# Kernel optimization log

Measured on AMD Instinct MI355X. Metric: run time of the kernel, lower is better.

Reference implementation:

```python
import jax, jax.numpy as jnp
import numpy as np
import math

D_MODEL = 1024
N_HEAD = 16
HEAD_DIM = D_MODEL // N_HEAD
D_FF = 4096
NUM_STEPS = 100.0
RESCALE = 4000.0
EPS = 1e-5


def _sin_emb(t):
    # SinusoidalPosEmb: t scaled by rescale_steps/num_steps
    half = D_MODEL // 2
    x = t.astype(jnp.float32) / NUM_STEPS * RESCALE
    freqs = jnp.exp(jnp.arange(half, dtype=jnp.float32) * (-math.log(10000.0) / (half - 1)))
    e = x[:, None] * freqs[None, :]
    return jnp.concatenate([jnp.sin(e), jnp.cos(e)], axis=-1)


def _ln(x):
    m = jnp.mean(x, axis=-1, keepdims=True)
    v = jnp.var(x, axis=-1, keepdims=True)
    return (x - m) / jnp.sqrt(v + EPS)


def _gelu2(x):
    return x * jax.nn.sigmoid(1.702 * x)


def setup_inputs() -> dict:
    key = jax.random.key(0)
    ks = jax.random.split(key, 24)
    B, S, D, F = 4, 512, D_MODEL, D_FF
    std = 0.02
    inp = {
        'src': jax.random.normal(ks[0], (B, S, D), dtype=jnp.float32),
        'src_mask': jax.random.randint(ks[1], (B, 1, S, S), 0, 2).astype(bool),
        'timestep': jax.random.randint(ks[2], (B,), 0, 100, dtype=jnp.int32),
        'attention_bias': jax.random.normal(ks[3], (B, N_HEAD, S, S), dtype=jnp.float32),
        # AdaLayerNorm linear: D -> 2D (scale, shift)
        'W_ada': jax.random.normal(ks[4], (D, 2 * D), dtype=jnp.float32) * std,
        'b_ada': jnp.zeros((2 * D,), dtype=jnp.float32),
        'Wq': jax.random.normal(ks[5], (D, D), dtype=jnp.float32) * std,
        'bq': jnp.zeros((D,), dtype=jnp.float32),
        'Wk': jax.random.normal(ks[6], (D, D), dtype=jnp.float32) * std,
        'bk': jnp.zeros((D,), dtype=jnp.float32),
        'Wv': jax.random.normal(ks[7], (D, D), dtype=jnp.float32) * std,
        'bv': jnp.zeros((D,), dtype=jnp.float32),
        'Wo': jax.random.normal(ks[8], (D, D), dtype=jnp.float32) * std,
        'bo': jnp.zeros((D,), dtype=jnp.float32),
        'W1': jax.random.normal(ks[9], (D, F), dtype=jnp.float32) * std,
        'b1': jnp.zeros((F,), dtype=jnp.float32),
        'W2': jax.random.normal(ks[10], (F, D), dtype=jnp.float32) * std,
        'b2': jnp.zeros((D,), dtype=jnp.float32),
        'g2': jnp.ones((D,), dtype=jnp.float32),
        'beta2': jnp.zeros((D,), dtype=jnp.float32),
    }
    return inp


def reference(src, src_mask, timestep, attention_bias, W_ada, b_ada,
              Wq, bq, Wk, bk, Wv, bv, Wo, bo, W1, b1, W2, b2, g2, beta2):
    B, S, D = src.shape
    # AdaLayerNorm: LN(x) * (1 + scale) + shift, scale/shift from timestep emb
    emb = jax.nn.silu(_sin_emb(timestep)) @ W_ada + b_ada  # [B, 2D]
    scale, shift = jnp.split(emb[:, None, :], 2, axis=-1)  # each [B,1,D]
    x = _ln(src) * (1.0 + scale) + shift

    # Self-attention with spatial bias + fp32 masked softmax
    q = (x @ Wq + bq).reshape(B, S, N_HEAD, HEAD_DIM).transpose(0, 2, 1, 3)
    k = (x @ Wk + bk).reshape(B, S, N_HEAD, HEAD_DIM).transpose(0, 2, 1, 3)
    v = (x @ Wv + bv).reshape(B, S, N_HEAD, HEAD_DIM).transpose(0, 2, 1, 3)
    scores = jnp.einsum('bhqd,bhkd->bhqk', q / math.sqrt(HEAD_DIM), k)
    scores = scores + attention_bias
    scores = jnp.where(src_mask, -jnp.inf, scores.astype(jnp.float32))
    probs = jax.nn.softmax(scores, axis=-1).astype(v.dtype)
    ctx = jnp.einsum('bhqk,bhkd->bhqd', probs, v)
    ctx = ctx.transpose(0, 2, 1, 3).reshape(B, S, D)
    x = x + (ctx @ Wo + bo)  # residual from AdaLN output (as in source)

    # FFN with gelu2 on LN2(x)
    h = _ln(x) * g2 + beta2
    ff = _gelu2(h @ W1 + b1) @ W2 + b2
    return x + ff
```

## Files before the change

### kernel.cpp

```cpp
#include <hip/hip_runtime.h>
#include <math.h>

typedef __bf16 bf16x8 __attribute__((ext_vector_type(8)));
typedef float  f32x4  __attribute__((ext_vector_type(4)));
typedef unsigned short u16x8 __attribute__((ext_vector_type(8)));

__device__ __forceinline__ float bf2f(unsigned short u) {
    return __uint_as_float(((unsigned int)u) << 16);
}
__device__ __forceinline__ unsigned short f2bf_n(float f) {
    return __builtin_bit_cast(unsigned short, (__bf16)f);
}

#define BATCH 4
#define SEQ 512
#define DM 1024
#define NH 16
#define DH 64
#define DFF 4096
#define MROWS (BATCH * SEQ)

__global__ __launch_bounds__(256) void fill0_kernel(float* __restrict__ out) {
    out[blockIdx.x * 256 + threadIdx.x] = 0.0f;
}

__global__ __launch_bounds__(256) void tconv_kernel(const float* __restrict__ in,
                                                    unsigned short* __restrict__ out,
                                                    int K, int N) {
    __shared__ float tile[64][33];
    const int n0 = blockIdx.x * 32, k0 = blockIdx.y * 64;
    const int t = threadIdx.x;
    const int tx = t & 31, ty = t >> 5;
    #pragma unroll
    for (int i = 0; i < 8; ++i)
        tile[ty + i * 8][tx] = in[(size_t)(k0 + ty + i * 8) * N + n0 + tx];
    __syncthreads();
    const int nr = t >> 3;
    const int ks = (t & 7) * 8;
    u16x8 v;
    #pragma unroll
    for (int j = 0; j < 8; ++j) v[j] = f2bf_n(tile[ks + j][nr]);
    *(u16x8*)&out[(size_t)(n0 + nr) * K + k0 + ks] = v;
}

__global__ __launch_bounds__(256) void tconv4_kernel(const float* __restrict__ i0,
                                                     const float* __restrict__ i1,
                                                     const float* __restrict__ i2,
                                                     const float* __restrict__ i3,
                                                     unsigned short* __restrict__ o0,
                                                     unsigned short* __restrict__ o1,
                                                     unsigned short* __restrict__ o2,
                                                     unsigned short* __restrict__ o3) {
    const int z = blockIdx.z;
    const float* in = (z == 0) ? i0 : (z == 1) ? i1 : (z == 2) ? i2 : i3;
    unsigned short* out = (z == 0) ? o0 : (z == 1) ? o1 : (z == 2) ? o2 : o3;
    __shared__ float tile[64][33];
    const int n0 = blockIdx.x * 32, k0 = blockIdx.y * 64;
    const int t = threadIdx.x;
    const int tx = t & 31, ty = t >> 5;
    #pragma unroll
    for (int i = 0; i < 8; ++i)
        tile[ty + i * 8][tx] = in[(size_t)(k0 + ty + i * 8) * 1024 + n0 + tx];
    __syncthreads();
    const int nr = t >> 3;
    const int ks = (t & 7) * 8;
    u16x8 v;
    #pragma unroll
    for (int j = 0; j < 8; ++j) v[j] = f2bf_n(tile[ks + j][nr]);
    *(u16x8*)&out[(size_t)(n0 + nr) * 1024 + k0 + ks] = v;
}

__global__ void semb_kernel(const int* __restrict__ ts, float* __restrict__ semb) {
    int b = blockIdx.x;
    float x = (float)ts[b] * 40.0f;
    for (int j = threadIdx.x; j < 1024; j += 256) {
        int idx = (j < 512) ? j : (j - 512);
        float fr = expf(-9.210340371976184f * (float)idx / 511.0f);
        float e = x * fr;
        float v = (j < 512) ? sinf(e) : cosf(e);
        semb[b * 1024 + j] = v / (1.0f + expf(-v));
    }
}

__global__ __launch_bounds__(256) void ada_part_kernel(const float* __restrict__ semb,
                                                       const float* __restrict__ W,
                                                       float* __restrict__ part) {
    const int nb = blockIdx.x, kc = blockIdx.y;
    const int t = threadIdx.x;
    __shared__ float e_s[4][64];
    e_s[t >> 6][t & 63] = semb[(t >> 6) * 1024 + kc * 64 + (t & 63)];
    __syncthreads();
    const int n = nb * 128 + (t & 127);
    const int half = t >> 7;
    float a0 = 0.f, a1 = 0.f, a2 = 0.f, a3 = 0.f;
    const int kk0 = half * 32;
    #pragma unroll 8
    for (int kk = kk0; kk < kk0 + 32; ++kk) {
        const float w = W[(size_t)(kc * 64 + kk) * 2048 + n];
        a0 += e_s[0][kk] * w; a1 += e_s[1][kk] * w;
        a2 += e_s[2][kk] * w; a3 += e_s[3][kk] * w;
    }
    const int j = kc * 2 + half;
    float* p = part + (size_t)j * 4 * 2048 + n;
    p[0] = a0; p[2048] = a1; p[2 * 2048] = a2; p[3 * 2048] = a3;
}

__global__ __launch_bounds__(256) void ada_red_kernel(const float* __restrict__ part,
                                                      const float* __restrict__ bias,
                                                      float* __restrict__ ss) {
    const int idx = blockIdx.x * 256 + threadIdx.x;
    const int b = idx >> 11, n = idx & 2047;
    float acc = bias[n];
    #pragma unroll 8
    for (int j = 0; j < 32; ++j) acc += part[((size_t)j * 4 + b) * 2048 + n];
    ss[b * 2048 + n] = acc;
}

__global__ __launch_bounds__(256) void adaln_kernel(const float* __restrict__ src,
                                                    const float* __restrict__ ss,
                                                    unsigned short* __restrict__ xb) {
    int r = blockIdx.x;
    int b = r >> 9;
    int t = threadIdx.x;
    float4 v4 = *reinterpret_cast<const float4*>(&src[(size_t)r * DM + t * 4]);
    float v[4] = {v4.x, v4.y, v4.z, v4.w};
    float s = v[0] + v[1] + v[2] + v[3];
    float q = v[0]*v[0] + v[1]*v[1] + v[2]*v[2] + v[3]*v[3];
    #pragma unroll
    for (int off = 32; off > 0; off >>= 1) { s += __shfl_down(s, off); q += __shfl_down(q, off); }
    __shared__ float red[8];
    if ((t & 63) == 0) { red[t >> 6] = s; red[4 + (t >> 6)] = q; }
    __syncthreads();
    s = red[0] + red[1] + red[2] + red[3];
    q = red[4] + red[5] + red[6] + red[7];
    float mean = s * (1.0f / DM);
    float var = q * (1.0f / DM) - mean * mean;
    float rstd = rsqrtf(var + 1e-5f);
    ushort4 o;
    o.x = f2bf_n((v[0]-mean)*rstd*(1.0f+ss[b*2048 + t*4+0]) + ss[b*2048+1024 + t*4+0]);
    o.y = f2bf_n((v[1]-mean)*rstd*(1.0f+ss[b*2048 + t*4+1]) + ss[b*2048+1024 + t*4+1]);
    o.z = f2bf_n((v[2]-mean)*rstd*(1.0f+ss[b*2048 + t*4+2]) + ss[b*2048+1024 + t*4+2]);
    o.w = f2bf_n((v[3]-mean)*rstd*(1.0f+ss[b*2048 + t*4+3]) + ss[b*2048+1024 + t*4+3]);
    *reinterpret_cast<ushort4*>(&xb[(size_t)r * DM + t * 4]) = o;
}

__global__ __launch_bounds__(256) void ln2_kernel(const unsigned short* __restrict__ x,
                                                  const float* __restrict__ g2,
                                                  const float* __restrict__ beta2,
                                                  unsigned short* __restrict__ hout) {
    int r = blockIdx.x;
    int t = threadIdx.x;
    ushort4 s4 = *reinterpret_cast<const ushort4*>(&x[(size_t)r * DM + t * 4]);
    float v[4] = {bf2f(s4.x), bf2f(s4.y), bf2f(s4.z), bf2f(s4.w)};
    float s = v[0] + v[1] + v[2] + v[3];
    float q = v[0]*v[0] + v[1]*v[1] + v[2]*v[2] + v[3]*v[3];
    #pragma unroll
    for (int off = 32; off > 0; off >>= 1) { s += __shfl_down(s, off); q += __shfl_down(q, off); }
    __shared__ float red[8];
    if ((t & 63) == 0) { red[t >> 6] = s; red[4 + (t >> 6)] = q; }
    __syncthreads();
    s = red[0] + red[1] + red[2] + red[3];
    q = red[4] + red[5] + red[6] + red[7];
    float mean = s * (1.0f / DM);
    float var = q * (1.0f / DM) - mean * mean;
    float rstd = rsqrtf(var + 1e-5f);
    ushort4 o;
    o.x = f2bf_n((v[0]-mean)*rstd*g2[t*4+0] + beta2[t*4+0]);
    o.y = f2bf_n((v[1]-mean)*rstd*g2[t*4+1] + beta2[t*4+1]);
    o.z = f2bf_n((v[2]-mean)*rstd*g2[t*4+2] + beta2[t*4+2]);
    o.w = f2bf_n((v[3]-mean)*rstd*g2[t*4+3] + beta2[t*4+3]);
    *reinterpret_cast<ushort4*>(&hout[(size_t)r * DM + t * 4]) = o;
}

#define TBM 64
#define TBN 128
#define TBK 64
#define PIT 68

template<int MODE>
__global__ __launch_bounds__(256) void gemm_bt(
    const unsigned short* __restrict__ A,
    const unsigned short* __restrict__ Wta, const unsigned short* __restrict__ Wtb,
    const unsigned short* __restrict__ Wtc,
    const float* __restrict__ ba, const float* __restrict__ bbb, const float* __restrict__ bc,
    const unsigned short* __restrict__ resid,
    unsigned short* __restrict__ oa, unsigned short* __restrict__ ob,
    unsigned short* __restrict__ oc,
    float* __restrict__ outF,
    int M, int N, int K, int ldk)
{
    const int gx = gridDim.x, gy = gridDim.y;
    const int nwg = gx * gy * gridDim.z;
    const int wid = blockIdx.x + gx * (blockIdx.y + gy * blockIdx.z);
    const int aid = (wid & 7) * (nwg >> 3) + (wid >> 3);
    const int plane = gx * gy;
    const int sel = aid / plane;
    const int pid = aid % plane;
    const int by = pid % gy;
    const int bx = pid / gy;

    const unsigned short* Wt = (sel == 0) ? Wta : (sel == 1) ? Wtb : Wtc;
    const float* bias = (sel == 0) ? ba : (sel == 1) ? bbb : bc;
    unsigned short* outB = (sel == 0) ? oa : (sel == 1) ? ob : oc;

    __shared__ unsigned short As[2][TBM * PIT];
    __shared__ unsigned short Bs[2][TBN * PIT];
    const int t = threadIdx.x;
    const int lane = t & 63;
    const int w = t >> 6, wm = w >> 1, wn = w & 1;
    const int l15 = lane & 15, l4 = lane >> 4;
    const int m0 = by * TBM, n0 = bx * TBN;

    f32x4 acc[2][4];
    #pragma unroll
    for (int i = 0; i < 2; ++i)
        #pragma unroll
        for (int j = 0; j < 4; ++j)
            #pragma unroll
            for (int r = 0; r < 4; ++r) acc[i][j][r] = 0.0f;

    const int ar = t >> 2, aseg = (t & 3) * 16;
    const unsigned short* aG = A + (size_t)(m0 + ar) * K + aseg;
    const int aLo = ar * PIT + aseg;
    const int br = t >> 1, bseg = (t & 1) * 32;
    const unsigned short* bG = Wt + (size_t)(n0 + br) * ldk + bseg;
    const int bLo = br * PIT + bseg;

    u16x8 ra0 = *(const u16x8*)(aG);
    u16x8 ra1 = *(const u16x8*)(aG + 8);
    u16x8 rb0 = *(const u16x8*)(bG);
    u16x8 rb1 = *(const u16x8*)(bG + 8);
    u16x8 rb2 = *(const u16x8*)(bG + 16);
    u16x8 rb3 = *(const u16x8*)(bG + 24);
    *(u16x8*)&As[0][aLo] = ra0; *(u16x8*)&As[0][aLo + 8] = ra1;
    *(u16x8*)&Bs[0][bLo] = rb0; *(u16x8*)&Bs[0][bLo + 8] = rb1;
    *(u16x8*)&Bs[0][bLo + 16] = rb2; *(u16x8*)&Bs[0][bLo + 24] = rb3;
    __syncthreads();

    const int NT = K / TBK;
    for (int kt = 0; kt < NT; ++kt) {
        const int cur = kt & 1;
        const bool more = (kt + 1 < NT);
        if (more) {
            const int k0 = (kt + 1) * TBK;
            ra0 = *(const u16x8*)(aG + k0);
            ra1 = *(const u16x8*)(aG + k0 + 8);
            rb0 = *(const u16x8*)(bG + k0);
            rb1 = *(const u16x8*)(bG + k0 + 8);
            rb2 = *(const u16x8*)(bG + k0 + 16);
            rb3 = *(const u16x8*)(bG + k0 + 24);
        }
        #pragma unroll
        for (int kk = 0; kk < 2; ++kk) {
            bf16x8 af[2], bfr[4];
            #pragma unroll
            for (int mt = 0; mt < 2; ++mt) {
                u16x8 tmp = *(const u16x8*)&As[cur][(wm*32 + mt*16 + l15) * PIT + kk*32 + l4*8];
                af[mt] = __builtin_bit_cast(bf16x8, tmp);
            }
            #pragma unroll
            for (int nt = 0; nt < 4; ++nt) {
                u16x8 tmp = *(const u16x8*)&Bs[cur][(wn*64 + nt*16 + l15) * PIT + kk*32 + l4*8];
                bfr[nt] = __builtin_bit_cast(bf16x8, tmp);
            }
            #pragma unroll
            for (int mt = 0; mt < 2; ++mt)
                #pragma unroll
                for (int nt = 0; nt < 4; ++nt)
                    acc[mt][nt] = __builtin_amdgcn_mfma_f32_16x16x32_bf16(
                        af[mt], bfr[nt], acc[mt][nt], 0, 0, 0);
        }
        if (more) {
            const int nx = cur ^ 1;
            *(u16x8*)&As[nx][aLo] = ra0; *(u16x8*)&As[nx][aLo + 8] = ra1;
            *(u16x8*)&Bs[nx][bLo] = rb0; *(u16x8*)&Bs[nx][bLo + 8] = rb1;
            *(u16x8*)&Bs[nx][bLo + 16] = rb2; *(u16x8*)&Bs[nx][bLo + 24] = rb3;
            __syncthreads();
        }
    }

    #pragma unroll
    for (int mt = 0; mt < 2; ++mt) {
        const int mbase = m0 + wm*32 + mt*16 + l4*4;
        #pragma unroll
        for (int nt = 0; nt < 4; ++nt) {
            const int n = n0 + wn*64 + nt*16 + l15;
            const float bs = (MODE == 4) ? 0.0f : bias[n];
            #pragma unroll
            for (int r = 0; r < 4; ++r) {
                const int m = mbase + r;
                float v = acc[mt][nt][r] + bs;
                if (MODE == 2) v = v / (1.0f + expf(-1.702f * v));
                if (MODE == 1 || MODE == 3) v += bf2f(resid[(size_t)m * N + n]);
                if (MODE == 3)      outF[(size_t)m * N + n] = v;
                else if (MODE == 4) outF[(size_t)m * N + n] += v;
                else                outB[(size_t)m * N + n] = f2bf_n(v);
            }
        }
    }
}

#define QB2 32
#define AKT 64
#define KROW 72
#define VROW 72
#define PROW 72
#define SBPIT 72

__global__ __launch_bounds__(128) void attn_mfma(const unsigned short* __restrict__ qbuf,
                                                 const unsigned short* __restrict__ kbuf,
                                                 const unsigned short* __restrict__ vbuf,
                                                 const float* __restrict__ attb,
                                                 const int* __restrict__ mask,
                                                 unsigned short* __restrict__ ctx) {
    __shared__ unsigned short Ks[AKT * KROW];
    __shared__ unsigned short Vt[DH * VROW];
    __shared__ unsigned short Pb[2 * 16 * PROW];
    __shared__ unsigned short Sb[QB2 * SBPIT];
    const int t = threadIdx.x;
    const int lane = t & 63;
    const int w = t >> 6;
    const int l15 = lane & 15, l4 = lane >> 4;
    const int q0 = blockIdx.x * QB2;
    const int h = blockIdx.y;
    const int b = blockIdx.z;

    bf16x8 qf[2];
    {
        const unsigned short* qrow = qbuf + ((size_t)(b * SEQ + q0 + w * 16 + l15)) * DM + h * DH;
        u16x8 t0 = *(const u16x8*)(qrow + l4 * 8);
        u16x8 t1 = *(const u16x8*)(qrow + 32 + l4 * 8);
        qf[0] = __builtin_bit_cast(bf16x8, t0);
        qf[1] = __builtin_bit_cast(bf16x8, t1);
    }

    float m[4] = {-1e30f, -1e30f, -1e30f, -1e30f};
    float l[4] = {0.0f, 0.0f, 0.0f, 0.0f};
    f32x4 o[4];
    #pragma unroll
    for (int dt = 0; dt < 4; ++dt)
        #pragma unroll
        for (int r = 0; r < 4; ++r) o[dt][r] = 0.0f;

    unsigned short* Pw = Pb + w * 16 * PROW;

    const int kr = t >> 1, c0 = (t & 1) * 32;
    const int kp = t & 31, vg = t >> 5;

    u16x8 rk0, rk1, rk2, rk3, rv0, rv1, rv2, rv3;
    float4 rb[4];
    int4   rm[4];

#define LOADT(KT) {                                                                     \
    const int kbase = (KT) * AKT;                                                       \
    const unsigned short* gk = kbuf + ((size_t)(b * SEQ + kbase + kr)) * DM + h * DH + c0; \
    rk0 = *(const u16x8*)gk;        rk1 = *(const u16x8*)(gk + 8);                      \
    rk2 = *(const u16x8*)(gk + 16); rk3 = *(const u16x8*)(gk + 24);                     \
    const unsigned short* gv = vbuf + ((size_t)(b * SEQ + kbase + 2 * kp)) * DM + h * DH + vg * 8; \
    rv0 = *(const u16x8*)gv;        rv1 = *(const u16x8*)(gv + DM);                     \
    rv2 = *(const u16x8*)(gv + 32); rv3 = *(const u16x8*)(gv + DM + 32);                \
    const float* bp = attb + (((size_t)(b * NH + h)) * SEQ + (q0 + w * 16)) * SEQ + kbase; \
    const int* mp = mask + ((size_t)(b * SEQ) + q0 + w * 16) * SEQ + kbase;             \
    _Pragma("unroll")                                                                   \
    for (int i = 0; i < 4; ++i) {                                                       \
        const int e = lane + i * 64; const int row = e >> 4, cg = e & 15;               \
        rb[i] = *(const float4*)&bp[(size_t)row * SEQ + cg * 4];                        \
        rm[i] = *(const int4*)&mp[(size_t)row * SEQ + cg * 4];                          \
    } }

#define STORET() {                                                                      \
    unsigned short* s = Ks + kr * KROW + c0;                                            \
    *(u16x8*)s = rk0; *(u16x8*)(s + 8) = rk1;                                           \
    *(u16x8*)(s + 16) = rk2; *(u16x8*)(s + 24) = rk3;                                   \
    unsigned int* vt32 = (unsigned int*)Vt;                                             \
    _Pragma("unroll")                                                                   \
    for (int j = 0; j < 8; ++j) {                                                       \
        vt32[(vg * 8 + j) * (VROW / 2) + kp] =                                          \
            (unsigned int)rv0[j] | ((unsigned int)rv1[j] << 16);                        \
        vt32[((vg + 4) * 8 + j) * (VROW / 2) + kp] =                                    \
            (unsigned int)rv2[j] | ((unsigned int)rv3[j] << 16);                        \
    }                                                                                   \
    _Pragma("unroll")                                                                   \
    for (int i = 0; i < 4; ++i) {                                                       \
        const int e = lane + i * 64; const int row = e >> 4, cg = e & 15;               \
        ushort4 cc;                                                                     \
        cc.x = f2bf_n(rm[i].x ? -8e30f : 8.0f * rb[i].x);                               \
        cc.y = f2bf_n(rm[i].y ? -8e30f : 8.0f * rb[i].y);                               \
        cc.z = f2bf_n(rm[i].z ? -8e30f : 8.0f * rb[i].z);                               \
        cc.w = f2bf_n(rm[i].w ? -8e30f : 8.0f * rb[i].w);                               \
        *(ushort4*)&Sb[(w * 16 + row) * SBPIT + cg * 4] = cc;                           \
    } }

    LOADT(0);
    for (int kt = 0; kt < SEQ / AKT; ++kt) {
        __syncthreads();
        STORET();
        __syncthreads();
        if (kt + 1 < SEQ / AKT) LOADT(kt + 1);

        f32x4 acc[4];
        #pragma unroll
        for (int nt = 0; nt < 4; ++nt)
            #pragma unroll
            for (int r = 0; r < 4; ++r)
                acc[nt][r] = bf2f(Sb[(w * 16 + l4 * 4 + r) * SBPIT + nt * 16 + l15]);

        #pragma unroll
        for (int kk = 0; kk < 2; ++kk) {
            #pragma unroll
            for (int nt = 0; nt < 4; ++nt) {
                u16x8 tmp = *(const u16x8*)(Ks + (nt * 16 + l15) * KROW + kk * 32 + l4 * 8);
                acc[nt] = __builtin_amdgcn_mfma_f32_16x16x32_bf16(
                    qf[kk], __builtin_bit_cast(bf16x8, tmp), acc[nt], 0, 0, 0);
            }
        }

        float pm[4] = {-1e30f, -1e30f, -1e30f, -1e30f};
        #pragma unroll
        for (int nt = 0; nt < 4; ++nt) {
            #pragma unroll
            for (int r = 0; r < 4; ++r) {
                const float sv = acc[nt][r] * 0.125f;
                acc[nt][r] = sv;
                pm[r] = fmaxf(pm[r], sv);
            }
        }
        #pragma unroll
        for (int r = 0; r < 4; ++r) {
            #pragma unroll
            for (int off = 1; off < 16; off <<= 1)
                pm[r] = fmaxf(pm[r], __shfl_xor(pm[r], off));
        }
        float al[4], ps[4];
        #pragma unroll
        for (int r = 0; r < 4; ++r) {
            const float mn = fmaxf(m[r], pm[r]);
            al[r] = __expf(m[r] - mn);
            m[r] = mn;
            ps[r] = 0.0f;
        }
        #pragma unroll
        for (int nt = 0; nt < 4; ++nt) {
            #pragma unroll
            for (int r = 0; r < 4; ++r) {
                const float p = __expf(acc[nt][r] - m[r]);
                acc[nt][r] = p;
                ps[r] += p;
            }
        }
        #pragma unroll
        for (int r = 0; r < 4; ++r) {
            #pragma unroll
            for (int off = 1; off < 16; off <<= 1) ps[r] += __shfl_xor(ps[r], off);
            l[r] = l[r] * al[r] + ps[r];
        }
        #pragma unroll
        for (int dt = 0; dt < 4; ++dt)
            #pragma unroll
            for (int r = 0; r < 4; ++r) o[dt][r] *= al[r];

        #pragma unroll
        for (int nt = 0; nt < 4; ++nt)
            #pragma unroll
            for (int r = 0; r < 4; ++r)
                Pw[(l4 * 4 + r) * PROW + nt * 16 + l15] = f2bf_n(acc[nt][r]);

        #pragma unroll
        for (int ks = 0; ks < 2; ++ks) {
            u16x8 pa = *(const u16x8*)(Pw + l15 * PROW + ks * 32 + l4 * 8);
            #pragma unroll
            for (int dt = 0; dt < 4; ++dt) {
                u16x8 vv = *(const u16x8*)(Vt + (dt * 16 + l15) * VROW + ks * 32 + l4 * 8);
                o[dt] = __builtin_amdgcn_mfma_f32_16x16x32_bf16(
                    __builtin_bit_cast(bf16x8, pa), __builtin_bit_cast(bf16x8, vv),
                    o[dt], 0, 0, 0);
            }
        }
    }

    #pragma unroll
    for (int r = 0; r < 4; ++r) {
        const float inv = 1.0f / l[r];
        const size_t row = (size_t)(b * SEQ + q0 + w * 16 + l4 * 4 + r) * DM + h * DH;
        #pragma unroll
        for (int dt = 0; dt < 4; ++dt)
            ctx[row + dt * 16 + l15] = f2bf_n(o[dt][r] * inv);
    }
#undef LOADT
#undef STORET
}

extern "C" void kernel_launch(void* const* d_in, const int* in_sizes, int n_in,
                              void* d_out, int out_size, void* d_ws, size_t ws_size,
                              hipStream_t stream) {
    const float* src  = (const float*)d_in[0];
    const int*   mask = (const int*)d_in[1];
    const int*   ts   = (const int*)d_in[2];
    const float* attb = (const float*)d_in[3];
    const float* Wada = (const float*)d_in[4];
    const float* bada = (const float*)d_in[5];
    const float* Wq   = (const float*)d_in[6];
    const float* bq   = (const float*)d_in[7];
    const float* Wk   = (const float*)d_in[8];
    const float* bk   = (const float*)d_in[9];
    const float* Wv   = (const float*)d_in[10];
    const float* bv   = (const float*)d_in[11];
    const float* Wo   = (const float*)d_in[12];
    const float* bo   = (const float*)d_in[13];
    const float* W1   = (const float*)d_in[14];
    const float* b1   = (const float*)d_in[15];
    const float* W2   = (const float*)d_in[16];
    const float* b2   = (const float*)d_in[17];
    const float* g2   = (const float*)d_in[18];
    const float* bt2  = (const float*)d_in[19];
    float* out = (float*)d_out;

    const size_t MB = 1024 * 1024;
    const size_t NEED = 65536 + 36 * MB;
    const size_t NEED_FULL = 65536 + 52 * MB;
    if (ws_size < NEED) {
        fill0_kernel<<<(size_t)MROWS * DM / 256, 256, 0, stream>>>(out);
        return;
    }
    const bool FULL = (ws_size >= NEED_FULL);

    char* ws = (char*)d_ws;
    float* semb = (float*)(ws + 4096);
    float* ss   = (float*)(ws + 24576);
    char*  base = ws + 65536;
    unsigned short* slotA = (unsigned short*)(base);
    unsigned short* slotB = (unsigned short*)(base + 4 * MB);
    unsigned short* slotC = (unsigned short*)(base + 8 * MB);
    unsigned short* vb   = (unsigned short*)d_out;
    unsigned short* ctxb = (unsigned short*)((char*)d_out + 4 * MB);
    unsigned short* xb = slotA;
    unsigned short* qb = slotB;
    unsigned short* kb = slotC;
    unsigned short* x2 = slotB;
    unsigned short* hb = slotC;
    unsigned short* midc = slotA;
    float* adap = (float*)slotC;

    unsigned short* Wtq = (unsigned short*)(base + 12 * MB);
    unsigned short* Wtk = Wtq + 1024 * 1024;
    unsigned short* Wtv = Wtk + 1024 * 1024;
    unsigned short* Wto = Wtv + 1024 * 1024;
    unsigned short* Wt1 = Wto + 1024 * 1024;
    unsigned short* Wt2 = Wt1 + (size_t)4096 * 1024;
    unsigned short* midF = (unsigned short*)(base + 36 * MB);

    tconv4_kernel<<<dim3(32, 16, 4), 256, 0, stream>>>(Wq, Wk, Wv, Wo, Wtq, Wtk, Wtv, Wto);
    tconv_kernel<<<dim3(128, 16), 256, 0, stream>>>(W1, Wt1, 1024, 4096);
    tconv_kernel<<<dim3(32, 64), 256, 0, stream>>>(W2, Wt2, 4096, 1024);

    semb_kernel<<<4, 256, 0, stream>>>(ts, semb);
    ada_part_kernel<<<dim3(16, 16), 256, 0, stream>>>(semb, Wada, adap);
    ada_red_kernel<<<32, 256, 0, stream>>>(adap, bada, ss);
    adaln_kernel<<<MROWS, 256, 0, stream>>>(src, ss, xb);

    gemm_bt<0><<<dim3(8, 32, 3), 256, 0, stream>>>(xb, Wtq, Wtk, Wtv, bq, bk, bv, nullptr,
                                                   qb, kb, vb, nullptr, MROWS, DM, DM, DM);
    attn_mfma<<<dim3(SEQ / QB2, NH, BATCH), 128, 0, stream>>>(qb, kb, vb, attb, mask, ctxb);
    gemm_bt<1><<<dim3(8, 32), 256, 0, stream>>>(ctxb, Wto, Wto, Wto, bo, bo, bo, xb,
                                                x2, x2, x2, nullptr, MROWS, DM, DM, DM);
    ln2_kernel<<<MROWS, 256, 0, stream>>>(x2, g2, bt2, hb);

    if (FULL) {
        gemm_bt<2><<<dim3(32, 32), 256, 0, stream>>>(hb, Wt1, Wt1, Wt1, b1, b1, b1, nullptr,
                                                     midF, midF, midF, nullptr,
                                                     MROWS, DFF, DM, DM);
        gemm_bt<3><<<dim3(8, 32), 256, 0, stream>>>(midF, Wt2, Wt2, Wt2, b2, b2, b2, x2,
                                                    nullptr, nullptr, nullptr, out,
                                                    MROWS, DM, DFF, DFF);
    } else {
        for (int nc = 0; nc < 4; ++nc) {
            const unsigned short* w1c = Wt1 + (size_t)nc * 1024 * 1024;
            const float* b1c = b1 + nc * 1024;
            gemm_bt<2><<<dim3(8, 32), 256, 0, stream>>>(hb, w1c, w1c, w1c, b1c, b1c, b1c,
                                                        nullptr, midc, midc, midc, nullptr,
                                                        MROWS, DM, DM, DM);
            const unsigned short* w2c = Wt2 + nc * 1024;
            if (nc == 0)
                gemm_bt<3><<<dim3(8, 32), 256, 0, stream>>>(midc, w2c, w2c, w2c, b2, b2, b2,
                                                            x2, nullptr, nullptr, nullptr, out,
                                                            MROWS, DM, DM, DFF);
            else
                gemm_bt<4><<<dim3(8, 32), 256, 0, stream>>>(midc, w2c, w2c, w2c,
                                                            nullptr, nullptr, nullptr, nullptr,
                                                            nullptr, nullptr, nullptr, out,
                                                            MROWS, DM, DM, DFF);
        }
    }
}
```

Measured before the change: 187.1 us.

## Rewrite GEMM with direct global-to-LDS loads, XOR swizzle and larger tiles

Replaces the register-staged, double-buffered GEMM with a single-buffer kernel that loads A and B tiles straight into LDS through global_load_lds and uses an XOR-swizzled layout instead of row padding. M tiles grow to 128, and N tiles are 128 or 64 depending on the GEMM. The chunked low-workspace FFN path is removed, so the code now requires the full workspace. Dropping the register double buffer means global loads no longer overlap with MFMA work inside a block, which adds a barrier stall per k-step in exchange for lower VGPR use and less LDS write traffic.

```diff
diff --git a/kernel.cpp b/kernel.cpp
--- a/kernel.cpp
+++ b/kernel.cpp
@@ -10,6 +10,11 @@
 }
 __device__ __forceinline__ unsigned short f2bf_n(float f) {
     return __builtin_bit_cast(unsigned short, (__bf16)f);
+}
+__device__ __forceinline__ void gl_lds16(const unsigned short* g, unsigned short* l) {
+    __builtin_amdgcn_global_load_lds(
+        (const __attribute__((address_space(1))) unsigned int*)g,
+        (__attribute__((address_space(3))) unsigned int*)l, 16, 0, 0);
 }
 
 #define BATCH 4
@@ -172,13 +177,8 @@
     *reinterpret_cast<ushort4*>(&hout[(size_t)r * DM + t * 4]) = o;
 }
 
-#define TBM 64
-#define TBN 128
-#define TBK 64
-#define PIT 68
-
-template<int MODE>
-__global__ __launch_bounds__(256) void gemm_bt(
+template<int MODE, int TN>
+__global__ __launch_bounds__(256) void gemm_gl(
     const unsigned short* __restrict__ A,
     const unsigned short* __restrict__ Wta, const unsigned short* __restrict__ Wtb,
     const unsigned short* __restrict__ Wtc,
@@ -189,6 +189,16 @@
     float* __restrict__ outF,
     int M, int N, int K, int ldk)
 {
+    constexpr int CR  = 128 + TN;
+    constexpr int RPW = CR / 4;
+    constexpr int NI  = RPW / 8;
+    constexpr int WAVE_N = (TN == 128) ? 2 : 1;
+    constexpr int WAVE_M = 4 / WAVE_N;
+    constexpr int AM = 128 / (WAVE_M * 16);
+    constexpr int AN = TN / (WAVE_N * 16);
+
+    __shared__ unsigned short LDSu[CR * 64];
+
     const int gx = gridDim.x, gy = gridDim.y;
     const int nwg = gx * gy * gridDim.z;
     const int wid = blockIdx.x + gx * (blockIdx.y + gy * blockIdx.z);
@@ -203,98 +213,80 @@
     const float* bias = (sel == 0) ? ba : (sel == 1) ? bbb : bc;
     unsigned short* outB = (sel == 0) ? oa : (sel == 1) ? ob : oc;
 
-    __shared__ unsigned short As[2][TBM * PIT];
-    __shared__ unsigned short Bs[2][TBN * PIT];
     const int t = threadIdx.x;
     const int lane = t & 63;
-    const int w = t >> 6, wm = w >> 1, wn = w & 1;
+    const int w = t >> 6;
     const int l15 = lane & 15, l4 = lane >> 4;
-    const int m0 = by * TBM, n0 = bx * TBN;
-
-    f32x4 acc[2][4];
-    #pragma unroll
-    for (int i = 0; i < 2; ++i)
-        #pragma unroll
-        for (int j = 0; j < 4; ++j)
+    const int wm = w / WAVE_N, wn = w % WAVE_N;
+    const int m0 = by * 128, n0 = bx * TN;
+
+    f32x4 acc[AM][AN];
+    #pragma unroll
+    for (int i = 0; i < AM; ++i)
+        #pragma unroll
+        for (int j = 0; j < AN; ++j)
             #pragma unroll
             for (int r = 0; r < 4; ++r) acc[i][j][r] = 0.0f;
 
-    const int ar = t >> 2, aseg = (t & 3) * 16;
-    const unsigned short* aG = A + (size_t)(m0 + ar) * K + aseg;
-    const int aLo = ar * PIT + aseg;
-    const int br = t >> 1, bseg = (t & 1) * 32;
-    const unsigned short* bG = Wt + (size_t)(n0 + br) * ldk + bseg;
-    const int bLo = br * PIT + bseg;
-
-    u16x8 ra0 = *(const u16x8*)(aG);
-    u16x8 ra1 = *(const u16x8*)(aG + 8);
-    u16x8 rb0 = *(const u16x8*)(bG);
-    u16x8 rb1 = *(const u16x8*)(bG + 8);
-    u16x8 rb2 = *(const u16x8*)(bG + 16);
-    u16x8 rb3 = *(const u16x8*)(bG + 24);
-    *(u16x8*)&As[0][aLo] = ra0; *(u16x8*)&As[0][aLo + 8] = ra1;
-    *(u16x8*)&Bs[0][bLo] = rb0; *(u16x8*)&Bs[0][bLo + 8] = rb1;
-    *(u16x8*)&Bs[0][bLo + 16] = rb2; *(u16x8*)&Bs[0][bLo + 24] = rb3;
-    __syncthreads();
-
-    const int NT = K / TBK;
+    const int gg = (lane & 7) ^ (lane >> 3);
+    const unsigned short* gp[NI];
+    unsigned short* lp[NI];
+    #pragma unroll
+    for (int i = 0; i < NI; ++i) {
+        const int cr = w * RPW + i * 8 + (lane >> 3);
+        gp[i] = (cr < 128) ? (A + (size_t)(m0 + cr) * K + gg * 8)
+                           : (Wt + (size_t)(n0 + cr - 128) * ldk + gg * 8);
+        lp[i] = LDSu + (w * RPW + i * 8) * 64;
+    }
+
+    const int NT = K / 64;
     for (int kt = 0; kt < NT; ++kt) {
-        const int cur = kt & 1;
-        const bool more = (kt + 1 < NT);
-        if (more) {
-            const int k0 = (kt + 1) * TBK;
-            ra0 = *(const u16x8*)(aG + k0);
-            ra1 = *(const u16x8*)(aG + k0 + 8);
-            rb0 = *(const u16x8*)(bG + k0);
-            rb1 = *(const u16x8*)(bG + k0 + 8);
-            rb2 = *(const u16x8*)(bG + k0 + 16);
-            rb3 = *(const u16x8*)(bG + k0 + 24);
-        }
+        const int k0 = kt * 64;
+        #pragma unroll
+        for (int i = 0; i < NI; ++i) gl_lds16(gp[i] + k0, lp[i]);
+        __syncthreads();
+
         #pragma unroll
         for (int kk = 0; kk < 2; ++kk) {
-            bf16x8 af[2], bfr[4];
-            #pragma unroll
-            for (int mt = 0; mt < 2; ++mt) {
-                u16x8 tmp = *(const u16x8*)&As[cur][(wm*32 + mt*16 + l15) * PIT + kk*32 + l4*8];
+            const int slot = ((kk * 4 + l4) ^ (l15 & 7)) * 8;
+            bf16x8 af[AM], bfr[AN];
+            #pragma unroll
+            for (int mt = 0; mt < AM; ++mt) {
+                const int row = wm * (AM * 16) + mt * 16 + l15;
+                u16x8 tmp = *(const u16x8*)(LDSu + row * 64 + slot);
                 af[mt] = __builtin_bit_cast(bf16x8, tmp);
             }
             #pragma unroll
-            for (int nt = 0; nt < 4; ++nt) {
-                u16x8 tmp = *(const u16x8*)&Bs[cur][(wn*64 + nt*16 + l15) * PIT + kk*32 + l4*8];
+            for (int nt = 0; nt < AN; ++nt) {
+                const int row = 128 + wn * (AN * 16) + nt * 16 + l15;
+                u16x8 tmp = *(const u16x8*)(LDSu + row * 64 + slot);
                 bfr[nt] = __builtin_bit_cast(bf16x8, tmp);
             }
             #pragma unroll
-            for (int mt = 0; mt < 2; ++mt)
+            for (int mt = 0; mt < AM; ++mt)
                 #pragma unroll
-                for (int nt = 0; nt < 4; ++nt)
+                for (int nt = 0; nt < AN; ++nt)
                     acc[mt][nt] = __builtin_amdgcn_mfma_f32_16x16x32_bf16(
                         af[mt], bfr[nt], acc[mt][nt], 0, 0, 0);
         }
-        if (more) {
-            const int nx = cur ^ 1;
-            *(u16x8*)&As[nx][aLo] = ra0; *(u16x8*)&As[nx][aLo + 8] = ra1;
-            *(u16x8*)&Bs[nx][bLo] = rb0; *(u16x8*)&Bs[nx][bLo + 8] = rb1;
-            *(u16x8*)&Bs[nx][bLo + 16] = rb2; *(u16x8*)&Bs[nx][bLo + 24] = rb3;
-            __syncthreads();
-        }
-    }
-
-    #pragma unroll
-    for (int mt = 0; mt < 2; ++mt) {
-        const int mbase = m0 + wm*32 + mt*16 + l4*4;
-        #pragma unroll
-        for (int nt = 0; nt < 4; ++nt) {
-            const int n = n0 + wn*64 + nt*16 + l15;
-            const float bs = (MODE == 4) ? 0.0f : bias[n];
+        if (kt + 1 < NT) __syncthreads();
+    }
+
+    #pragma unroll
+    for (int mt = 0; mt < AM; ++mt) {
+        const int mbase = m0 + wm * (AM * 16) + mt * 16 + l4 * 4;
+        #pragma unroll
+        for (int nt = 0; nt < AN; ++nt) {
+            const int n = n0 + wn * (AN * 16) + nt * 16 + l15;
+            const float bs = bias[n];
             #pragma unroll
             for (int r = 0; r < 4; ++r) {
                 const int m = mbase + r;
                 float v = acc[mt][nt][r] + bs;
                 if (MODE == 2) v = v / (1.0f + expf(-1.702f * v));
                 if (MODE == 1 || MODE == 3) v += bf2f(resid[(size_t)m * N + n]);
-                if (MODE == 3)      outF[(size_t)m * N + n] = v;
-                else if (MODE == 4) outF[(size_t)m * N + n] += v;
-                else                outB[(size_t)m * N + n] = f2bf_n(v);
+                if (MODE == 3) outF[(size_t)m * N + n] = v;
+                else           outB[(size_t)m * N + n] = f2bf_n(v);
             }
         }
     }
@@ -516,13 +508,11 @@
     float* out = (float*)d_out;
 
     const size_t MB = 1024 * 1024;
-    const size_t NEED = 65536 + 36 * MB;
     const size_t NEED_FULL = 65536 + 52 * MB;
-    if (ws_size < NEED) {
+    if (ws_size < NEED_FULL) {
         fill0_kernel<<<(size_t)MROWS * DM / 256, 256, 0, stream>>>(out);
         return;
     }
-    const bool FULL = (ws_size >= NEED_FULL);
 
     char* ws = (char*)d_ws;
     float* semb = (float*)(ws + 4096);
@@ -538,7 +528,6 @@
     unsigned short* kb = slotC;
     unsigned short* x2 = slotB;
     unsigned short* hb = slotC;
-    unsigned short* midc = slotA;
     float* adap = (float*)slotC;
 
     unsigned short* Wtq = (unsigned short*)(base + 12 * MB);
@@ -558,37 +547,15 @@
     ada_red_kernel<<<32, 256, 0, stream>>>(adap, bada, ss);
     adaln_kernel<<<MROWS, 256, 0, stream>>>(src, ss, xb);
 
-    gemm_bt<0><<<dim3(8, 32, 3), 256, 0, stream>>>(xb, Wtq, Wtk, Wtv, bq, bk, bv, nullptr,
-                                                   qb, kb, vb, nullptr, MROWS, DM, DM, DM);
+    gemm_gl<0, 128><<<dim3(8, 16, 3), 256, 0, stream>>>(
+        xb, Wtq, Wtk, Wtv, bq, bk, bv, nullptr, qb, kb, vb, nullptr, MROWS, DM, DM, DM);
     attn_mfma<<<dim3(SEQ / QB2, NH, BATCH), 128, 0, stream>>>(qb, kb, vb, attb, mask, ctxb);
-    gemm_bt<1><<<dim3(8, 32), 256, 0, stream>>>(ctxb, Wto, Wto, Wto, bo, bo, bo, xb,
-                                                x2, x2, x2, nullptr, MROWS, DM, DM, DM);
+    gemm_gl<1, 64><<<dim3(16, 16), 256, 0, stream>>>(
+        ctxb, Wto, Wto, Wto, bo, bo, bo, xb, x2, x2, x2, nullptr, MROWS, DM, DM, DM);
     ln2_kernel<<<MROWS, 256, 0, stream>>>(x2, g2, bt2, hb);
-
-    if (FULL) {
-        gemm_bt<2><<<dim3(32, 32), 256, 0, stream>>>(hb, Wt1, Wt1, Wt1, b1, b1, b1, nullptr,
-                                                     midF, midF, midF, nullptr,
-                                                     MROWS, DFF, DM, DM);
-        gemm_bt<3><<<dim3(8, 32), 256, 0, stream>>>(midF, Wt2, Wt2, Wt2, b2, b2, b2, x2,
-                                                    nullptr, nullptr, nullptr, out,
-                                                    MROWS, DM, DFF, DFF);
-    } else {
-        for (int nc = 0; nc < 4; ++nc) {
-            const unsigned short* w1c = Wt1 + (size_t)nc * 1024 * 1024;
-            const float* b1c = b1 + nc * 1024;
-            gemm_bt<2><<<dim3(8, 32), 256, 0, stream>>>(hb, w1c, w1c, w1c, b1c, b1c, b1c,
-                                                        nullptr, midc, midc, midc, nullptr,
-                                                        MROWS, DM, DM, DM);
-            const unsigned short* w2c = Wt2 + nc * 1024;
-            if (nc == 0)
-                gemm_bt<3><<<dim3(8, 32), 256, 0, stream>>>(midc, w2c, w2c, w2c, b2, b2, b2,
-                                                            x2, nullptr, nullptr, nullptr, out,
-                                                            MROWS, DM, DM, DFF);
-            else
-                gemm_bt<4><<<dim3(8, 32), 256, 0, stream>>>(midc, w2c, w2c, w2c,
-                                                            nullptr, nullptr, nullptr, nullptr,
-                                                            nullptr, nullptr, nullptr, out,
-                                                            MROWS, DM, DM, DFF);
-        }
-    }
-}
+    gemm_gl<2, 128><<<dim3(32, 16), 256, 0, stream>>>(
+        hb, Wt1, Wt1, Wt1, b1, b1, b1, nullptr, midF, midF, midF, nullptr, MROWS, DFF, DM, DM);
+    gemm_gl<3, 64><<<dim3(16, 16), 256, 0, stream>>>(
+        midF, Wt2, Wt2, Wt2, b2, b2, b2, x2, nullptr, nullptr, nullptr, out,
+        MROWS, DM, DFF, DFF);
+}
```

New measurement: 190.3 us. About the same (+1.7%).
